# Optimization experiments

Hardware: AMD Instinct MI355X
Metric: run time of the kernel (lower is better)

## Reference

```python
import jax, jax.numpy as jnp
import numpy as np
import math

IN_DIM = 768
FREQ = IN_DIM // 2 + 1          # 385
K = max(1, int(FREQ * 0.1))     # 38
MLP_IN = 2 * K                  # 76
HID = 256
LN_EPS = 1e-5


def _spectral_mask(task_id=0):
    # Faithful port of PiNoiseBiLoRA._get_spectral_mask
    avail = np.arange(1, FREQ)
    mt = 20
    idx = avail[task_id % mt::mt]
    if len(idx) >= K:
        idx = idx[:K]
    else:
        needed = K - len(idx)
        rf = math.ceil(needed / len(idx))
        idx = np.concatenate([idx, np.tile(idx, rf)[:needed]])
    return idx.astype(np.int32)


def setup_inputs() -> dict:
    key = jax.random.key(0)
    ks = jax.random.split(key, 6)
    B, S = 8, 4096
    x = jax.random.normal(ks[0], (B, S, IN_DIM), dtype=jnp.float32)
    eps = jax.random.normal(ks[1], (B, S, MLP_IN), dtype=jnp.float32)
    indices = jnp.asarray(_spectral_mask(0))
    w_scale = 0.05
    mu_w1 = jax.random.normal(ks[2], (HID, MLP_IN), dtype=jnp.float32) * w_scale
    mu_w2 = jax.random.normal(ks[3], (MLP_IN, HID), dtype=jnp.float32) * w_scale
    sg_w1 = jax.random.normal(ks[4], (HID, MLP_IN), dtype=jnp.float32) * w_scale
    sg_w2 = jax.random.normal(ks[5], (MLP_IN, HID), dtype=jnp.float32) * w_scale
    zeros_h = jnp.zeros((HID,), jnp.float32)
    zeros_o = jnp.zeros((MLP_IN,), jnp.float32)
    ones_h = jnp.ones((HID,), jnp.float32)
    return {
        'x': x, 'eps': eps, 'indices': indices,
        'mu_w1': mu_w1, 'mu_b1': zeros_h, 'mu_g': ones_h, 'mu_beta': zeros_h,
        'mu_w2': mu_w2, 'mu_b2': zeros_o,
        'sg_w1': sg_w1, 'sg_b1': zeros_h, 'sg_g': ones_h, 'sg_beta': zeros_h,
        'sg_w2': sg_w2, 'sg_b2': zeros_o,
    }


def _mlp(x, w1, b1, g, beta, w2, b2):
    # Linear -> LayerNorm -> GELU(exact) -> Linear
    h = x @ w1.T + b1
    mu = h.mean(axis=-1, keepdims=True)
    var = jnp.mean((h - mu) ** 2, axis=-1, keepdims=True)
    h = (h - mu) * jax.lax.rsqrt(var + LN_EPS) * g + beta
    h = jax.nn.gelu(h, approximate=False)
    return h @ w2.T + b2


def reference(x, eps, indices,
              mu_w1, mu_b1, mu_g, mu_beta, mu_w2, mu_b2,
              sg_w1, sg_b1, sg_g, sg_beta, sg_w2, sg_b2):
    # Training-mode forward of PiNoiseBiLoRA
    x_freq = jnp.fft.rfft(x, axis=-1)            # [B,S,FREQ] complex64
    x_sel = x_freq[..., indices]                 # gather k freq bins
    x_in = jnp.concatenate([x_sel.real, x_sel.imag], axis=-1)  # [B,S,2k]
    mu = _mlp(x_in, mu_w1, mu_b1, mu_g, mu_beta, mu_w2, mu_b2)
    sigma = _mlp(x_in, sg_w1, sg_b1, sg_g, sg_beta, sg_w2, sg_b2)
    z = mu + eps * sigma                         # reparameterization
    z_complex = jax.lax.complex(z[..., :K], z[..., K:]).astype(jnp.complex64)
    noise = jnp.zeros(x_freq.shape, jnp.complex64).at[..., indices].add(z_complex)
    return jnp.fft.irfft(noise, n=IN_DIM, axis=-1)
```

## Files before the change

kernel.cpp:

```cpp
#include <hip/hip_runtime.h>
#include <hip/hip_bf16.h>
#include <math.h>

#define INDIM 768
#define NROWS 32768
#define KSEL  38
#define NCOLS 76
#define HID   256
#define LN_EPS 1e-5f

typedef float  f32x4  __attribute__((ext_vector_type(4)));
typedef __bf16 bf16x8 __attribute__((ext_vector_type(8)));

#define MFMA16(a,b,c) __builtin_amdgcn_mfma_f32_16x16x32_bf16((a),(b),(c),0,0,0)

#define OFF_BFP 0
#define OFF_W1P 122880
#define OFF_W2P 221184
#define OFF_BSP 303104

__global__ void k_prep(const int* __restrict__ idxs,
                       const float* __restrict__ mu_w1, const float* __restrict__ sg_w1,
                       const float* __restrict__ mu_w2, const float* __restrict__ sg_w2,
                       __bf16* __restrict__ BfP, __bf16* __restrict__ W1P,
                       __bf16* __restrict__ W2P, __bf16* __restrict__ BsP)
{
    int tid = blockIdx.x * blockDim.x + threadIdx.x;
    int nth = gridDim.x * blockDim.x;
    const float TH = 6.28318530717958647692f / (float)INDIM;

    for (int e = tid; e < 120 * 512; e += nth) {
        int frag = e >> 9, lane = (e >> 3) & 63, j = e & 7;
        int kc = frag / 5, nt = frag % 5;
        int c = nt * 16 + (lane & 15);
        int k = kc * 32 + ((lane >> 4) << 3) + j;
        float v = 0.f;
        if (c < NCOLS) {
            int cc = (c < KSEL) ? c : c - KSEL;
            int f = idxs[cc];
            int m = (f * k) % INDIM;
            float s, co; sincosf(TH * (float)m, &s, &co);
            v = (c < KSEL) ? co : -s;
        }
        BfP[e] = (__bf16)v;
    }
    for (int e = tid; e < 96 * 512; e += nth) {
        int frag = e >> 9, lane = (e >> 3) & 63, j = e & 7;
        int mlp = frag / 48; int r = frag % 48;
        int nt = r / 3, ks = r % 3;
        int row = nt * 16 + (lane & 15);
        int k = ks * 32 + ((lane >> 4) << 3) + j;
        const float* W = mlp ? sg_w1 : mu_w1;
        W1P[e] = (__bf16)((k < NCOLS) ? W[row * NCOLS + k] : 0.f);
    }
    for (int e = tid; e < 80 * 512; e += nth) {
        int frag = e >> 9, lane = (e >> 3) & 63, j = e & 7;
        int mlp = frag / 40; int r = frag % 40;
        int nt = r / 8, ks = r % 8;
        int row = nt * 16 + (lane & 15);
        int k = ks * 32 + ((lane >> 4) << 3) + j;
        const float* W = mlp ? sg_w2 : mu_w2;
        W2P[e] = (__bf16)((row < NCOLS) ? W[row * HID + k] : 0.f);
    }
    for (int e = tid; e < 144 * 512; e += nth) {
        int frag = e >> 9, lane = (e >> 3) & 63, j = e & 7;
        int nt = frag / 3, ks = frag % 3;
        int n = nt * 16 + (lane & 15);
        int k = ks * 32 + ((lane >> 4) << 3) + j;
        float v = 0.f;
        if (k < NCOLS) {
            int cc = (k < KSEL) ? k : k - KSEL;
            int f = idxs[cc];
            int m = (f * n) % INDIM;
            float s, co; sincosf(TH * (float)m, &s, &co);
            v = ((k < KSEL) ? co : -s) * (2.0f / (float)INDIM);
        }
        BsP[e] = (__bf16)v;
    }
}

static __device__ inline float gelu_fast(float v) {
    float u = v * (0.79788456080286535588f + 0.03567740813636141f * v * v);
    return v / (1.f + __expf(-2.f * u));
}

static __device__ __forceinline__ void stage16(
    const __bf16* __restrict__ src, int nunits, char* dst, int w, int lane)
{
    typedef __attribute__((address_space(1))) const unsigned int g_u32;
    typedef __attribute__((address_space(3))) unsigned int l_u32;
    for (int u = w; u < nunits; u += 16)
        __builtin_amdgcn_global_load_lds((g_u32*)(src + (size_t)u * 512 + lane * 8),
                                         (l_u32*)(dst + u * 1024), 16, 0, 0);
}

__global__ __launch_bounds__(1024, 4) void k_fused(
    const float* __restrict__ x, const float* __restrict__ eps,
    const __bf16* __restrict__ Bf, const __bf16* __restrict__ W1f,
    const __bf16* __restrict__ W2f, const __bf16* __restrict__ Bs,
    const float* __restrict__ mu_b1, const float* __restrict__ mu_g,
    const float* __restrict__ mu_be, const float* __restrict__ mu_b2,
    const float* __restrict__ sg_b1, const float* __restrict__ sg_g,
    const float* __restrict__ sg_be, const float* __restrict__ sg_b2,
    float* __restrict__ out)
{
    __shared__ __align__(16) char   R[122880];
    __shared__ __align__(16) __bf16 tbuf[8][1664];
    float* PA = (float*)R;

    int tid = threadIdx.x;
    int w = tid >> 6, lane = tid & 63, q = lane >> 4, l16 = lane & 15;
    int t = w >> 1, p = w & 1;
    int rbase = blockIdx.x * 128 + t * 16;

    f32x4 acc[5] = {};
    {
        const float* xrow = x + (size_t)(rbase + l16) * INDIM + p * 384 + q * 8;
        stage16(Bf, 120, R, w, lane);
        float4 f0 = ((const float4*)xrow)[0];
        float4 f1 = ((const float4*)xrow)[1];
        __syncthreads();
        #pragma unroll
        for (int kk = 0; kk < 12; ++kk) {
            float4 n0, n1;
            if (kk < 11) {
                n0 = ((const float4*)(xrow + (kk + 1) * 32))[0];
                n1 = ((const float4*)(xrow + (kk + 1) * 32))[1];
            }
            union { __bf16 h[8]; bf16x8 v; } a;
            a.h[0]=(__bf16)f0.x; a.h[1]=(__bf16)f0.y; a.h[2]=(__bf16)f0.z; a.h[3]=(__bf16)f0.w;
            a.h[4]=(__bf16)f1.x; a.h[5]=(__bf16)f1.y; a.h[6]=(__bf16)f1.z; a.h[7]=(__bf16)f1.w;
            const char* bb = R + (size_t)((p * 12 + kk) * 5) * 1024 + (size_t)lane * 16;
            #pragma unroll
            for (int nt = 0; nt < 5; ++nt) {
                bf16x8 b = *(const bf16x8*)(bb + nt * 1024);
                acc[nt] = MFMA16(a.v, b, acc[nt]);
            }
            if (kk < 11) { f0 = n0; f1 = n1; }
        }
    }
    __syncthreads();
    if (p == 1) {
        #pragma unroll
        for (int nt = 0; nt < 5; ++nt)
            #pragma unroll
            for (int r = 0; r < 4; ++r)
                PA[t * 1280 + (q * 4 + r) * 80 + nt * 16 + l16] = acc[nt][r];
    }
    __syncthreads();
    if (p == 0) {
        #pragma unroll
        for (int nt = 0; nt < 5; ++nt)
            #pragma unroll
            for (int r = 0; r < 4; ++r) {
                float v = acc[nt][r] + PA[t * 1280 + (q * 4 + r) * 80 + nt * 16 + l16];
                tbuf[t][(q * 4 + r) * 104 + nt * 16 + l16] = (__bf16)v;
            }
        #pragma unroll
        for (int r = 0; r < 4; ++r)
            tbuf[t][(q * 4 + r) * 104 + 80 + l16] = (__bf16)0.f;
    }
    __syncthreads();
    bf16x8 a1[3];
    #pragma unroll
    for (int ks = 0; ks < 3; ++ks)
        a1[ks] = *(const bf16x8*)&tbuf[t][l16 * 104 + ks * 32 + q * 8];
    stage16(W1f, 96, R, w, lane);
    __syncthreads();

    const float* b1 = p ? sg_b1 : mu_b1;
    const float* g  = p ? sg_g  : mu_g;
    const float* be = p ? sg_be : mu_be;

    f32x4 h[16] = {};
    #pragma unroll
    for (int nt = 0; nt < 16; ++nt)
        #pragma unroll
        for (int ks = 0; ks < 3; ++ks) {
            bf16x8 b = *(const bf16x8*)(R + (size_t)((p * 48 + nt * 3 + ks) * 1024)
                                          + (size_t)lane * 16);
            h[nt] = MFMA16(a1[ks], b, h[nt]);
        }
    float s[4] = {}, ss[4] = {};
    #pragma unroll
    for (int nt = 0; nt < 16; ++nt) {
        float bb = b1[nt * 16 + l16];
        #pragma unroll
        for (int r = 0; r < 4; ++r) {
            float v = h[nt][r] + bb; h[nt][r] = v;
            s[r] += v; ss[r] += v * v;
        }
    }
    #pragma unroll
    for (int off = 1; off < 16; off <<= 1)
        #pragma unroll
        for (int r = 0; r < 4; ++r) {
            s[r] += __shfl_xor(s[r], off); ss[r] += __shfl_xor(ss[r], off);
        }
    float mean[4], rstd[4];
    #pragma unroll
    for (int r = 0; r < 4; ++r) {
        mean[r] = s[r] * (1.f / 256.f);
        rstd[r] = rsqrtf(ss[r] * (1.f / 256.f) - mean[r] * mean[r] + LN_EPS);
    }
    __syncthreads();
    __bf16* gw = (__bf16*)R + w * 2176;
    bf16x8 a2[8];
    #pragma unroll
    for (int half = 0; half < 2; ++half) {
        #pragma unroll
        for (int ntl = 0; ntl < 8; ++ntl) {
            int nt = half * 8 + ntl;
            int i = nt * 16 + l16;
            float gv = g[i], bev = be[i];
            #pragma unroll
            for (int r = 0; r < 4; ++r)
                gw[(q * 4 + r) * 136 + ntl * 16 + l16] =
                    (__bf16)gelu_fast((h[nt][r] - mean[r]) * rstd[r] * gv + bev);
        }
        #pragma unroll
        for (int ks = 0; ks < 4; ++ks)
            a2[half * 4 + ks] = *(const bf16x8*)&gw[l16 * 136 + ks * 32 + q * 8];
    }
    __syncthreads();
    stage16(W2f, 80, R, w, lane);
    __syncthreads();

    f32x4 o[5] = {};
    #pragma unroll
    for (int nt = 0; nt < 5; ++nt)
        #pragma unroll
        for (int ks = 0; ks < 8; ++ks) {
            bf16x8 b = *(const bf16x8*)(R + (size_t)((p * 40 + nt * 8 + ks) * 1024)
                                          + (size_t)lane * 16);
            o[nt] = MFMA16(a2[ks], b, o[nt]);
        }
    __syncthreads();

    float ev[5][4];
    if (p == 0) {
        #pragma unroll
        for (int nt = 0; nt < 5; ++nt)
            #pragma unroll
            for (int r = 0; r < 4; ++r)
                PA[t * 1280 + (q * 4 + r) * 80 + nt * 16 + l16] = o[nt][r];
    } else {
        #pragma unroll
        for (int nt = 0; nt < 5; ++nt) {
            int j = nt * 16 + l16;
            #pragma unroll
            for (int r = 0; r < 4; ++r)
                ev[nt][r] = (j < NCOLS)
                    ? eps[(size_t)(rbase + q * 4 + r) * NCOLS + j] : 0.f;
        }
    }
    __syncthreads();
    if (p == 1) {
        #pragma unroll
        for (int nt = 0; nt < 5; ++nt) {
            int j = nt * 16 + l16;
            float b2m = (j < NCOLS) ? mu_b2[j] : 0.f;
            float b2s = (j < NCOLS) ? sg_b2[j] : 0.f;
            #pragma unroll
            for (int r = 0; r < 4; ++r) {
                float z = 0.f;
                if (j < NCOLS) {
                    float omu = PA[t * 1280 + (q * 4 + r) * 80 + j];
                    z = (omu + b2m) + ev[nt][r] * (o[nt][r] + b2s);
                }
                tbuf[t][(q * 4 + r) * 104 + j] = (__bf16)z;
            }
        }
        #pragma unroll
        for (int r = 0; r < 4; ++r)
            tbuf[t][(q * 4 + r) * 104 + 80 + l16] = (__bf16)0.f;
    }
    __syncthreads();
    bf16x8 az[3];
    #pragma unroll
    for (int ks = 0; ks < 3; ++ks)
        az[ks] = *(const bf16x8*)&tbuf[t][l16 * 104 + ks * 32 + q * 8];
    stage16(Bs, 72, R, w, lane);
    __syncthreads();

    #pragma unroll
    for (int half = 0; half < 2; ++half) {
        if (half == 1) {
            __syncthreads();
            stage16(Bs + (size_t)72 * 512, 72, R, w, lane);
            __syncthreads();
        }
        #pragma unroll 4
        for (int c = 0; c < 12; ++c) {
            int ntl = p * 12 + c;
            int nt  = half * 24 + ntl;
            f32x4 oc = {};
            #pragma unroll
            for (int ks = 0; ks < 3; ++ks) {
                bf16x8 b = *(const bf16x8*)(R + (size_t)((ntl * 3 + ks) * 1024)
                                              + (size_t)lane * 16);
                oc = MFMA16(az[ks], b, oc);
            }
            #pragma unroll
            for (int r = 0; r < 4; ++r)
                out[(size_t)(rbase + q * 4 + r) * INDIM + nt * 16 + l16] = oc[r];
        }
    }
}

extern "C" void kernel_launch(void* const* d_in, const int* in_sizes, int n_in,
                              void* d_out, int out_size, void* d_ws, size_t ws_size,
                              hipStream_t stream)
{
    const float* x     = (const float*)d_in[0];
    const float* eps   = (const float*)d_in[1];
    const int*   idxs  = (const int*)  d_in[2];
    const float* mu_w1 = (const float*)d_in[3];
    const float* mu_b1 = (const float*)d_in[4];
    const float* mu_g  = (const float*)d_in[5];
    const float* mu_be = (const float*)d_in[6];
    const float* mu_w2 = (const float*)d_in[7];
    const float* mu_b2 = (const float*)d_in[8];
    const float* sg_w1 = (const float*)d_in[9];
    const float* sg_b1 = (const float*)d_in[10];
    const float* sg_g  = (const float*)d_in[11];
    const float* sg_be = (const float*)d_in[12];
    const float* sg_w2 = (const float*)d_in[13];
    const float* sg_b2 = (const float*)d_in[14];
    float* out = (float*)d_out;

    char* ws = (char*)d_ws;
    __bf16* BfP = (__bf16*)(ws + OFF_BFP);
    __bf16* W1P = (__bf16*)(ws + OFF_W1P);
    __bf16* W2P = (__bf16*)(ws + OFF_W2P);
    __bf16* BsP = (__bf16*)(ws + OFF_BSP);

    hipLaunchKernelGGL(k_prep, dim3(1024), dim3(256), 0, stream,
                       idxs, mu_w1, sg_w1, mu_w2, sg_w2, BfP, W1P, W2P, BsP);
    hipLaunchKernelGGL(k_fused, dim3(NROWS / 128), dim3(1024), 0, stream,
                       x, eps, BfP, W1P, W2P, BsP,
                       mu_b1, mu_g, mu_be, mu_b2,
                       sg_b1, sg_g, sg_be, sg_b2, out);
}
```

Baseline: 235.7 us.

## Halve block size and double-buffer weight staging in LDS across all GEMM phases

Shrinks each block from 1024 threads and 128 rows to 512 threads and 64 rows, cutting LDS from about 150KB to about 77KB so more blocks can share a CU. Weight matrices are no longer staged whole; they stream in chunks through two 32KB LDS buffers, with the next chunk's async global-to-LDS copy issued while MFMAs run on the current one. The W1 and Bs stage-ins are moved ahead of unrelated work to hide load latency. In exchange the kernel has many more barriers per block and reloads the weights twice as often across the grid.

```diff
diff --git a/kernel.cpp b/kernel.cpp
--- a/kernel.cpp
+++ b/kernel.cpp
@@ -84,17 +84,21 @@
     return v / (1.f + __expf(-2.f * u));
 }
 
-static __device__ __forceinline__ void stage16(
-    const __bf16* __restrict__ src, int nunits, char* dst, int w, int lane)
+static __device__ __forceinline__ void stage8(
+    const __bf16* __restrict__ s0, const __bf16* __restrict__ s1,
+    int nkb, char* dst, int w, int lane)
 {
     typedef __attribute__((address_space(1))) const unsigned int g_u32;
     typedef __attribute__((address_space(3))) unsigned int l_u32;
-    for (int u = w; u < nunits; u += 16)
-        __builtin_amdgcn_global_load_lds((g_u32*)(src + (size_t)u * 512 + lane * 8),
+    for (int u = w; u < 2 * nkb; u += 8) {
+        const __bf16* s = (u < nkb) ? (s0 + (size_t)u * 512)
+                                    : (s1 + (size_t)(u - nkb) * 512);
+        __builtin_amdgcn_global_load_lds((g_u32*)(s + lane * 8),
                                          (l_u32*)(dst + u * 1024), 16, 0, 0);
-}
-
-__global__ __launch_bounds__(1024, 4) void k_fused(
+    }
+}
+
+__global__ __launch_bounds__(512, 4) void k_fused(
     const float* __restrict__ x, const float* __restrict__ eps,
     const __bf16* __restrict__ Bf, const __bf16* __restrict__ W1f,
     const __bf16* __restrict__ W2f, const __bf16* __restrict__ Bs,
@@ -104,42 +108,50 @@
     const float* __restrict__ sg_be, const float* __restrict__ sg_b2,
     float* __restrict__ out)
 {
-    __shared__ __align__(16) char   R[122880];
-    __shared__ __align__(16) __bf16 tbuf[8][1664];
-    float* PA = (float*)R;
+    __shared__ __align__(16) char   R[65536];
+    __shared__ __align__(16) __bf16 tbuf[4][1664];
+    float* PA = (float*)(R + 45056);
 
     int tid = threadIdx.x;
     int w = tid >> 6, lane = tid & 63, q = lane >> 4, l16 = lane & 15;
     int t = w >> 1, p = w & 1;
-    int rbase = blockIdx.x * 128 + t * 16;
+    int rbase = blockIdx.x * 64 + t * 16;
 
     f32x4 acc[5] = {};
     {
         const float* xrow = x + (size_t)(rbase + l16) * INDIM + p * 384 + q * 8;
-        stage16(Bf, 120, R, w, lane);
+        stage8(Bf, Bf + (size_t)60 * 512, 15, R, w, lane);
         float4 f0 = ((const float4*)xrow)[0];
         float4 f1 = ((const float4*)xrow)[1];
         __syncthreads();
         #pragma unroll
-        for (int kk = 0; kk < 12; ++kk) {
-            float4 n0, n1;
-            if (kk < 11) {
-                n0 = ((const float4*)(xrow + (kk + 1) * 32))[0];
-                n1 = ((const float4*)(xrow + (kk + 1) * 32))[1];
-            }
-            union { __bf16 h[8]; bf16x8 v; } a;
-            a.h[0]=(__bf16)f0.x; a.h[1]=(__bf16)f0.y; a.h[2]=(__bf16)f0.z; a.h[3]=(__bf16)f0.w;
-            a.h[4]=(__bf16)f1.x; a.h[5]=(__bf16)f1.y; a.h[6]=(__bf16)f1.z; a.h[7]=(__bf16)f1.w;
-            const char* bb = R + (size_t)((p * 12 + kk) * 5) * 1024 + (size_t)lane * 16;
-            #pragma unroll
-            for (int nt = 0; nt < 5; ++nt) {
-                bf16x8 b = *(const bf16x8*)(bb + nt * 1024);
-                acc[nt] = MFMA16(a.v, b, acc[nt]);
-            }
-            if (kk < 11) { f0 = n0; f1 = n1; }
-        }
-    }
-    __syncthreads();
+        for (int c = 0; c < 4; ++c) {
+            if (c < 3)
+                stage8(Bf + (size_t)(15 * (c + 1)) * 512,
+                       Bf + (size_t)(60 + 15 * (c + 1)) * 512,
+                       15, R + ((c & 1) ^ 1) * 32768, w, lane);
+            const char* cb = R + (c & 1) * 32768 + p * 15360 + (size_t)lane * 16;
+            #pragma unroll
+            for (int kkl = 0; kkl < 3; ++kkl) {
+                int kk = c * 3 + kkl;
+                float4 n0, n1;
+                if (kk < 11) {
+                    n0 = ((const float4*)(xrow + (kk + 1) * 32))[0];
+                    n1 = ((const float4*)(xrow + (kk + 1) * 32))[1];
+                }
+                union { __bf16 h[8]; bf16x8 v; } a;
+                a.h[0]=(__bf16)f0.x; a.h[1]=(__bf16)f0.y; a.h[2]=(__bf16)f0.z; a.h[3]=(__bf16)f0.w;
+                a.h[4]=(__bf16)f1.x; a.h[5]=(__bf16)f1.y; a.h[6]=(__bf16)f1.z; a.h[7]=(__bf16)f1.w;
+                #pragma unroll
+                for (int nt = 0; nt < 5; ++nt) {
+                    bf16x8 b = *(const bf16x8*)(cb + (kkl * 5 + nt) * 1024);
+                    acc[nt] = MFMA16(a.v, b, acc[nt]);
+                }
+                if (kk < 11) { f0 = n0; f1 = n1; }
+            }
+            __syncthreads();
+        }
+    }
     if (p == 1) {
         #pragma unroll
         for (int nt = 0; nt < 5; ++nt)
@@ -148,6 +160,7 @@
                 PA[t * 1280 + (q * 4 + r) * 80 + nt * 16 + l16] = acc[nt][r];
     }
     __syncthreads();
+    stage8(W1f, W1f + (size_t)48 * 512, 12, R, w, lane);
     if (p == 0) {
         #pragma unroll
         for (int nt = 0; nt < 5; ++nt)
@@ -165,8 +178,6 @@
     #pragma unroll
     for (int ks = 0; ks < 3; ++ks)
         a1[ks] = *(const bf16x8*)&tbuf[t][l16 * 104 + ks * 32 + q * 8];
-    stage16(W1f, 96, R, w, lane);
-    __syncthreads();
 
     const float* b1 = p ? sg_b1 : mu_b1;
     const float* g  = p ? sg_g  : mu_g;
@@ -174,13 +185,21 @@
 
     f32x4 h[16] = {};
     #pragma unroll
-    for (int nt = 0; nt < 16; ++nt)
-        #pragma unroll
-        for (int ks = 0; ks < 3; ++ks) {
-            bf16x8 b = *(const bf16x8*)(R + (size_t)((p * 48 + nt * 3 + ks) * 1024)
-                                          + (size_t)lane * 16);
-            h[nt] = MFMA16(a1[ks], b, h[nt]);
-        }
+    for (int c = 0; c < 4; ++c) {
+        if (c < 3)
+            stage8(W1f + (size_t)(12 * (c + 1)) * 512,
+                   W1f + (size_t)(48 + 12 * (c + 1)) * 512,
+                   12, R + ((c & 1) ^ 1) * 32768, w, lane);
+        const char* cb = R + (c & 1) * 32768 + p * 12288 + (size_t)lane * 16;
+        #pragma unroll
+        for (int ntl = 0; ntl < 4; ++ntl)
+            #pragma unroll
+            for (int ks = 0; ks < 3; ++ks) {
+                bf16x8 b = *(const bf16x8*)(cb + (ntl * 3 + ks) * 1024);
+                h[4 * c + ntl] = MFMA16(a1[ks], b, h[4 * c + ntl]);
+            }
+        __syncthreads();
+    }
     float s[4] = {}, ss[4] = {};
     #pragma unroll
     for (int nt = 0; nt < 16; ++nt) {
@@ -203,7 +222,6 @@
         mean[r] = s[r] * (1.f / 256.f);
         rstd[r] = rsqrtf(ss[r] * (1.f / 256.f) - mean[r] * mean[r] + LN_EPS);
     }
-    __syncthreads();
     __bf16* gw = (__bf16*)R + w * 2176;
     bf16x8 a2[8];
     #pragma unroll
@@ -223,20 +241,34 @@
             a2[half * 4 + ks] = *(const bf16x8*)&gw[l16 * 136 + ks * 32 + q * 8];
     }
     __syncthreads();
-    stage16(W2f, 80, R, w, lane);
-    __syncthreads();
-
+
+    stage8(W2f, W2f + (size_t)40 * 512, 16, R, w, lane);
+    __syncthreads();
     f32x4 o[5] = {};
     #pragma unroll
-    for (int nt = 0; nt < 5; ++nt)
-        #pragma unroll
-        for (int ks = 0; ks < 8; ++ks) {
-            bf16x8 b = *(const bf16x8*)(R + (size_t)((p * 40 + nt * 8 + ks) * 1024)
-                                          + (size_t)lane * 16);
-            o[nt] = MFMA16(a2[ks], b, o[nt]);
-        }
-    __syncthreads();
-
+    for (int c = 0; c < 3; ++c) {
+        if (c < 2) {
+            int nkbn = (c == 1) ? 8 : 16;
+            stage8(W2f + (size_t)(16 * (c + 1)) * 512,
+                   W2f + (size_t)(40 + 16 * (c + 1)) * 512,
+                   nkbn, R + ((c & 1) ^ 1) * 32768, w, lane);
+        }
+        int nkb = (c == 2) ? 8 : 16;
+        int ntn = (c == 2) ? 1 : 2;
+        const char* cb = R + (c & 1) * 32768 + p * (nkb * 1024) + (size_t)lane * 16;
+        #pragma unroll
+        for (int ntl = 0; ntl < 2; ++ntl) {
+            if (ntl >= ntn) break;
+            #pragma unroll
+            for (int ks = 0; ks < 8; ++ks) {
+                bf16x8 b = *(const bf16x8*)(cb + (ntl * 8 + ks) * 1024);
+                o[2 * c + ntl] = MFMA16(a2[ks], b, o[2 * c + ntl]);
+            }
+        }
+        __syncthreads();
+    }
+
+    stage8(Bs, Bs + (size_t)72 * 512, 12, R, w, lane);
     float ev[5][4];
     if (p == 0) {
         #pragma unroll
@@ -280,31 +312,28 @@
     #pragma unroll
     for (int ks = 0; ks < 3; ++ks)
         az[ks] = *(const bf16x8*)&tbuf[t][l16 * 104 + ks * 32 + q * 8];
-    stage16(Bs, 72, R, w, lane);
-    __syncthreads();
-
-    #pragma unroll
-    for (int half = 0; half < 2; ++half) {
-        if (half == 1) {
-            __syncthreads();
-            stage16(Bs + (size_t)72 * 512, 72, R, w, lane);
-            __syncthreads();
-        }
-        #pragma unroll 4
-        for (int c = 0; c < 12; ++c) {
-            int ntl = p * 12 + c;
-            int nt  = half * 24 + ntl;
+
+    #pragma unroll
+    for (int c = 0; c < 6; ++c) {
+        if (c < 5)
+            stage8(Bs + (size_t)(12 * (c + 1)) * 512,
+                   Bs + (size_t)(72 + 12 * (c + 1)) * 512,
+                   12, R + ((c & 1) ^ 1) * 32768, w, lane);
+        const char* cb = R + (c & 1) * 32768 + p * 12288 + (size_t)lane * 16;
+        #pragma unroll
+        for (int ntl = 0; ntl < 4; ++ntl) {
+            int nt = p * 24 + 4 * c + ntl;
             f32x4 oc = {};
             #pragma unroll
             for (int ks = 0; ks < 3; ++ks) {
-                bf16x8 b = *(const bf16x8*)(R + (size_t)((ntl * 3 + ks) * 1024)
-                                              + (size_t)lane * 16);
+                bf16x8 b = *(const bf16x8*)(cb + (ntl * 3 + ks) * 1024);
                 oc = MFMA16(az[ks], b, oc);
             }
             #pragma unroll
             for (int r = 0; r < 4; ++r)
                 out[(size_t)(rbase + q * 4 + r) * INDIM + nt * 16 + l16] = oc[r];
         }
+        if (c < 5) __syncthreads();
     }
 }
 
@@ -337,7 +366,7 @@
 
     hipLaunchKernelGGL(k_prep, dim3(1024), dim3(256), 0, stream,
                        idxs, mu_w1, sg_w1, mu_w2, sg_w2, BfP, W1P, W2P, BsP);
-    hipLaunchKernelGGL(k_fused, dim3(NROWS / 128), dim3(1024), 0, stream,
+    hipLaunchKernelGGL(k_fused, dim3(NROWS / 64), dim3(512), 0, stream,
                        x, eps, BfP, W1P, W2P, BsP,
                        mu_b1, mu_g, mu_be, mu_b2,
                        sg_b1, sg_g, sg_be, sg_b2, out);
```

Measured after the change: 237.0 us. About the same (+0.6%).

## Split forward and inverse DFT GEMMs across four K-quarters with two row tiles per wave

Applied to the files above, without the earlier changes.

The forward DFT projection and the inverse DFT output GEMM are re-partitioned. Each wave now handles two 16-row tiles over a quarter of the K range (forward) or a quarter of the output columns (inverse), so every B fragment read from LDS feeds two MFMAs. The forward partial sums are reduced through LDS across four K-quarters instead of two, and the x register prefetch double-buffering is dropped. The aim is less LDS bandwidth per MFMA and more independent MFMA chains, at the cost of more accumulator registers and a larger cross-wave reduction.

```diff
diff --git a/kernel.cpp b/kernel.cpp
--- a/kernel.cpp
+++ b/kernel.cpp
@@ -106,66 +106,83 @@
 {
     __shared__ __align__(16) char   R[122880];
     __shared__ __align__(16) __bf16 tbuf[8][1664];
-    float* PA = (float*)R;
+    float* PA3 = (float*)R;
+    float* PA  = (float*)R;
 
     int tid = threadIdx.x;
     int w = tid >> 6, lane = tid & 63, q = lane >> 4, l16 = lane & 15;
-    int t = w >> 1, p = w & 1;
-    int rbase = blockIdx.x * 128 + t * 16;
-
-    f32x4 acc[5] = {};
+    int pr = w >> 2, kq = w & 3;
+    int t0 = pr, t1 = pr + 4;
+    int rb0 = blockIdx.x * 128 + t0 * 16;
+    int rb1 = blockIdx.x * 128 + t1 * 16;
+    int t2 = w >> 1, p = w & 1;
+    int rbase2 = blockIdx.x * 128 + t2 * 16;
+
+    f32x4 acc0[5] = {}, acc1[5] = {};
     {
-        const float* xrow = x + (size_t)(rbase + l16) * INDIM + p * 384 + q * 8;
+        const float* xr0 = x + (size_t)(rb0 + l16) * INDIM + kq * 192 + q * 8;
+        const float* xr1 = xr0 + (size_t)64 * INDIM;
         stage16(Bf, 120, R, w, lane);
-        float4 f0 = ((const float4*)xrow)[0];
-        float4 f1 = ((const float4*)xrow)[1];
         __syncthreads();
         #pragma unroll
-        for (int kk = 0; kk < 12; ++kk) {
-            float4 n0, n1;
-            if (kk < 11) {
-                n0 = ((const float4*)(xrow + (kk + 1) * 32))[0];
-                n1 = ((const float4*)(xrow + (kk + 1) * 32))[1];
-            }
-            union { __bf16 h[8]; bf16x8 v; } a;
-            a.h[0]=(__bf16)f0.x; a.h[1]=(__bf16)f0.y; a.h[2]=(__bf16)f0.z; a.h[3]=(__bf16)f0.w;
-            a.h[4]=(__bf16)f1.x; a.h[5]=(__bf16)f1.y; a.h[6]=(__bf16)f1.z; a.h[7]=(__bf16)f1.w;
-            const char* bb = R + (size_t)((p * 12 + kk) * 5) * 1024 + (size_t)lane * 16;
+        for (int kk = 0; kk < 6; ++kk) {
+            float4 f0 = ((const float4*)(xr0 + kk * 32))[0];
+            float4 f1 = ((const float4*)(xr0 + kk * 32))[1];
+            float4 g0 = ((const float4*)(xr1 + kk * 32))[0];
+            float4 g1 = ((const float4*)(xr1 + kk * 32))[1];
+            union { __bf16 h[8]; bf16x8 v; } a0, a1u;
+            a0.h[0]=(__bf16)f0.x; a0.h[1]=(__bf16)f0.y; a0.h[2]=(__bf16)f0.z; a0.h[3]=(__bf16)f0.w;
+            a0.h[4]=(__bf16)f1.x; a0.h[5]=(__bf16)f1.y; a0.h[6]=(__bf16)f1.z; a0.h[7]=(__bf16)f1.w;
+            a1u.h[0]=(__bf16)g0.x; a1u.h[1]=(__bf16)g0.y; a1u.h[2]=(__bf16)g0.z; a1u.h[3]=(__bf16)g0.w;
+            a1u.h[4]=(__bf16)g1.x; a1u.h[5]=(__bf16)g1.y; a1u.h[6]=(__bf16)g1.z; a1u.h[7]=(__bf16)g1.w;
+            const char* bb = R + (size_t)((kq * 6 + kk) * 5) * 1024 + (size_t)lane * 16;
             #pragma unroll
             for (int nt = 0; nt < 5; ++nt) {
                 bf16x8 b = *(const bf16x8*)(bb + nt * 1024);
-                acc[nt] = MFMA16(a.v, b, acc[nt]);
-            }
-            if (kk < 11) { f0 = n0; f1 = n1; }
-        }
-    }
-    __syncthreads();
-    if (p == 1) {
+                acc0[nt] = MFMA16(a0.v, b, acc0[nt]);
+                acc1[nt] = MFMA16(a1u.v, b, acc1[nt]);
+            }
+        }
+    }
+    __syncthreads();
+    if (kq != 0) {
+        int base0 = ((kq - 1) * 8 + t0) * 1280;
+        int base1 = ((kq - 1) * 8 + t1) * 1280;
         #pragma unroll
         for (int nt = 0; nt < 5; ++nt)
             #pragma unroll
-            for (int r = 0; r < 4; ++r)
-                PA[t * 1280 + (q * 4 + r) * 80 + nt * 16 + l16] = acc[nt][r];
-    }
-    __syncthreads();
-    if (p == 0) {
+            for (int r = 0; r < 4; ++r) {
+                int i = (q * 4 + r) * 80 + nt * 16 + l16;
+                PA3[base0 + i] = acc0[nt][r];
+                PA3[base1 + i] = acc1[nt][r];
+            }
+    }
+    __syncthreads();
+    if (kq == 0) {
         #pragma unroll
         for (int nt = 0; nt < 5; ++nt)
             #pragma unroll
             for (int r = 0; r < 4; ++r) {
-                float v = acc[nt][r] + PA[t * 1280 + (q * 4 + r) * 80 + nt * 16 + l16];
-                tbuf[t][(q * 4 + r) * 104 + nt * 16 + l16] = (__bf16)v;
-            }
-        #pragma unroll
-        for (int r = 0; r < 4; ++r)
-            tbuf[t][(q * 4 + r) * 104 + 80 + l16] = (__bf16)0.f;
-    }
-    __syncthreads();
+                int i = (q * 4 + r) * 80 + nt * 16 + l16;
+                float v0 = acc0[nt][r] + PA3[t0 * 1280 + i]
+                         + PA3[(8 + t0) * 1280 + i] + PA3[(16 + t0) * 1280 + i];
+                float v1 = acc1[nt][r] + PA3[t1 * 1280 + i]
+                         + PA3[(8 + t1) * 1280 + i] + PA3[(16 + t1) * 1280 + i];
+                tbuf[t0][(q * 4 + r) * 104 + nt * 16 + l16] = (__bf16)v0;
+                tbuf[t1][(q * 4 + r) * 104 + nt * 16 + l16] = (__bf16)v1;
+            }
+        #pragma unroll
+        for (int r = 0; r < 4; ++r) {
+            tbuf[t0][(q * 4 + r) * 104 + 80 + l16] = (__bf16)0.f;
+            tbuf[t1][(q * 4 + r) * 104 + 80 + l16] = (__bf16)0.f;
+        }
+    }
+    __syncthreads();
+    stage16(W1f, 96, R, w, lane);
     bf16x8 a1[3];
     #pragma unroll
     for (int ks = 0; ks < 3; ++ks)
-        a1[ks] = *(const bf16x8*)&tbuf[t][l16 * 104 + ks * 32 + q * 8];
-    stage16(W1f, 96, R, w, lane);
+        a1[ks] = *(const bf16x8*)&tbuf[t2][l16 * 104 + ks * 32 + q * 8];
     __syncthreads();
 
     const float* b1 = p ? sg_b1 : mu_b1;
@@ -243,7 +260,7 @@
         for (int nt = 0; nt < 5; ++nt)
             #pragma unroll
             for (int r = 0; r < 4; ++r)
-                PA[t * 1280 + (q * 4 + r) * 80 + nt * 16 + l16] = o[nt][r];
+                PA[t2 * 1280 + (q * 4 + r) * 80 + nt * 16 + l16] = o[nt][r];
     } else {
         #pragma unroll
         for (int nt = 0; nt < 5; ++nt) {
@@ -251,7 +268,7 @@
             #pragma unroll
             for (int r = 0; r < 4; ++r)
                 ev[nt][r] = (j < NCOLS)
-                    ? eps[(size_t)(rbase + q * 4 + r) * NCOLS + j] : 0.f;
+                    ? eps[(size_t)(rbase2 + q * 4 + r) * NCOLS + j] : 0.f;
         }
     }
     __syncthreads();
@@ -265,22 +282,24 @@
             for (int r = 0; r < 4; ++r) {
                 float z = 0.f;
                 if (j < NCOLS) {
-                    float omu = PA[t * 1280 + (q * 4 + r) * 80 + j];
+                    float omu = PA[t2 * 1280 + (q * 4 + r) * 80 + j];
                     z = (omu + b2m) + ev[nt][r] * (o[nt][r] + b2s);
                 }
-                tbuf[t][(q * 4 + r) * 104 + j] = (__bf16)z;
+                tbuf[t2][(q * 4 + r) * 104 + j] = (__bf16)z;
             }
         }
         #pragma unroll
         for (int r = 0; r < 4; ++r)
-            tbuf[t][(q * 4 + r) * 104 + 80 + l16] = (__bf16)0.f;
-    }
-    __syncthreads();
-    bf16x8 az[3];
-    #pragma unroll
-    for (int ks = 0; ks < 3; ++ks)
-        az[ks] = *(const bf16x8*)&tbuf[t][l16 * 104 + ks * 32 + q * 8];
+            tbuf[t2][(q * 4 + r) * 104 + 80 + l16] = (__bf16)0.f;
+    }
+    __syncthreads();
     stage16(Bs, 72, R, w, lane);
+    bf16x8 az0[3], az1[3];
+    #pragma unroll
+    for (int ks = 0; ks < 3; ++ks) {
+        az0[ks] = *(const bf16x8*)&tbuf[t0][l16 * 104 + ks * 32 + q * 8];
+        az1[ks] = *(const bf16x8*)&tbuf[t1][l16 * 104 + ks * 32 + q * 8];
+    }
     __syncthreads();
 
     #pragma unroll
@@ -290,20 +309,23 @@
             stage16(Bs + (size_t)72 * 512, 72, R, w, lane);
             __syncthreads();
         }
-        #pragma unroll 4
-        for (int c = 0; c < 12; ++c) {
-            int ntl = p * 12 + c;
-            int nt  = half * 24 + ntl;
-            f32x4 oc = {};
+        #pragma unroll 3
+        for (int c = 0; c < 6; ++c) {
+            int ntl = kq * 6 + c;
+            int ntg = half * 24 + ntl;
+            f32x4 oc0 = {}, oc1 = {};
             #pragma unroll
             for (int ks = 0; ks < 3; ++ks) {
                 bf16x8 b = *(const bf16x8*)(R + (size_t)((ntl * 3 + ks) * 1024)
                                               + (size_t)lane * 16);
-                oc = MFMA16(az[ks], b, oc);
-            }
-            #pragma unroll
-            for (int r = 0; r < 4; ++r)
-                out[(size_t)(rbase + q * 4 + r) * INDIM + nt * 16 + l16] = oc[r];
+                oc0 = MFMA16(az0[ks], b, oc0);
+                oc1 = MFMA16(az1[ks], b, oc1);
+            }
+            #pragma unroll
+            for (int r = 0; r < 4; ++r) {
+                out[(size_t)(rb0 + q * 4 + r) * INDIM + ntg * 16 + l16] = oc0[r];
+                out[(size_t)(rb1 + q * 4 + r) * INDIM + ntg * 16 + l16] = oc1[r];
+            }
         }
     }
 }
```

Result: slower. 243.8 us (+3.4%).
